# Optimization experiments

Hardware: AMD Instinct MI355X
Metric: run time of the kernel (lower is better)

The kernel has to match this reference:

```python
import math
import jax, jax.numpy as jnp
import numpy as np

N_HEAD = 8
BLOCK_SIZE = 1024
LN_EPS = 1e-5


def _layer_norm(x, g, b):
    mu = jnp.mean(x, axis=-1, keepdims=True)
    var = jnp.var(x, axis=-1, keepdims=True)
    return (x - mu) * jax.lax.rsqrt(var + LN_EPS) * g + b


def _skew(QEr):
    # QEr: (B, nh, L, L) -> pad one zero column on the left, reshape, drop first row
    B, nh, nr, nc = QEr.shape
    padded = jnp.pad(QEr, ((0, 0), (0, 0), (0, 0), (1, 0)))  # (B, nh, nr, nc+1)
    reshaped = padded.reshape(B, nh, nc + 1, nr)
    return reshaped[:, :, 1:, :]  # (B, nh, nr, nc)


def _attn(x, W_qkv, b_qkv, W_o, b_o, Er):
    B, L, D = x.shape
    hs = D // N_HEAD
    qkv = x @ W_qkv + b_qkv  # (B, L, 3D)
    q, k, v = jnp.split(qkv, 3, axis=-1)
    # (B, nh, L, hs)
    q = q.reshape(B, L, N_HEAD, hs).transpose(0, 2, 1, 3)
    k = k.reshape(B, L, N_HEAD, hs).transpose(0, 2, 1, 3)
    v = v.reshape(B, L, N_HEAD, hs).transpose(0, 2, 1, 3)
    start = BLOCK_SIZE - L
    Er_t = Er[start:, :].T  # (hs, L)
    QEr = q @ Er_t  # (B, nh, L, L)
    Srel = _skew(QEr)
    scores = (jnp.einsum('bhqd,bhkd->bhqk', q, k) + Srel) * (1.0 / math.sqrt(hs))
    causal = jnp.tril(jnp.ones((L, L), dtype=bool))
    scores = jnp.where(causal, scores, jnp.float32(-jnp.inf))
    att = jax.nn.softmax(scores, axis=-1)
    y = jnp.einsum('bhqk,bhkd->bhqd', att, v)
    y = y.transpose(0, 2, 1, 3).reshape(B, L, D)
    return y @ W_o + b_o


def reference(x, W_qkv, b_qkv, W_o, b_o, Er, ln1_g, ln1_b, ln2_g, ln2_b,
              W_fc, b_fc, W_proj, b_proj):
    x = x + _attn(_layer_norm(x, ln1_g, ln1_b), W_qkv, b_qkv, W_o, b_o, Er)
    h = _layer_norm(x, ln2_g, ln2_b) @ W_fc + b_fc
    h = jax.nn.gelu(h, approximate=False)
    h = h @ W_proj + b_proj
    return x + h


def setup_inputs() -> dict:
    key = jax.random.key(0)
    ks = jax.random.split(key, 8)
    B, L, D, F = 8, 1024, 1024, 4096
    hs = D // N_HEAD
    s = lambda fan_in: 1.0 / math.sqrt(fan_in)
    return {
        'x': jax.random.normal(ks[0], (B, L, D), dtype=jnp.float32),
        'W_qkv': jax.random.normal(ks[1], (D, 3 * D), dtype=jnp.float32) * s(D),
        'b_qkv': jnp.zeros((3 * D,), dtype=jnp.float32),
        'W_o': jax.random.normal(ks[2], (D, D), dtype=jnp.float32) * s(D),
        'b_o': jnp.zeros((D,), dtype=jnp.float32),
        'Er': jax.random.normal(ks[3], (BLOCK_SIZE, hs), dtype=jnp.float32),
        'ln1_g': jnp.ones((D,), dtype=jnp.float32),
        'ln1_b': jnp.zeros((D,), dtype=jnp.float32),
        'ln2_g': jnp.ones((D,), dtype=jnp.float32),
        'ln2_b': jnp.zeros((D,), dtype=jnp.float32),
        'W_fc': jax.random.normal(ks[4], (D, F), dtype=jnp.float32) * s(D),
        'b_fc': jnp.zeros((F,), dtype=jnp.float32),
        'W_proj': jax.random.normal(ks[5], (F, D), dtype=jnp.float32) * s(F),
        'b_proj': jnp.zeros((D,), dtype=jnp.float32),
    }
```

## Files before the change

kernel.cpp:

```cpp
#include <hip/hip_runtime.h>
#include <hip/hip_bf16.h>
#include <math.h>

#define BB 8
#define LL 1024
#define DD 1024
#define FF 4096
#define NHH 8
#define HSS 128
#define SCALE 0.08838834764831845f
#define TRI(qi, kt) ((qi) * ((qi) + 1) / 2 + (kt))

typedef __bf16 bf16;
typedef __bf16 bf16x8 __attribute__((ext_vector_type(8)));
typedef float f32x4 __attribute__((ext_vector_type(4)));
typedef _Float16 f16;
typedef _Float16 f16x4 __attribute__((ext_vector_type(4)));

__device__ inline void async_copy16(const void* g, void* l) {
  __builtin_amdgcn_global_load_lds(
      (const __attribute__((address_space(1))) unsigned int*)g,
      (__attribute__((address_space(3))) unsigned int*)l, 16, 0, 0);
}

__global__ __launch_bounds__(256)
void transpose_cast_kernel(const float* __restrict__ W, bf16* __restrict__ Wt,
                           int K, int N) {
  __shared__ float tile[32][33];
  int n0 = blockIdx.x * 32, k0 = blockIdx.y * 32;
  int tx = threadIdx.x, ty = threadIdx.y;
#pragma unroll
  for (int i = 0; i < 32; i += 8)
    tile[ty + i][tx] = W[(size_t)(k0 + ty + i) * N + n0 + tx];
  __syncthreads();
#pragma unroll
  for (int i = 0; i < 32; i += 8)
    Wt[(size_t)(n0 + ty + i) * K + k0 + tx] = (bf16)tile[tx][ty + i];
}

__global__ __launch_bounds__(256)
void cast_bf16_kernel(const float* __restrict__ src, bf16* __restrict__ dst, int n) {
  int i = blockIdx.x * blockDim.x + threadIdx.x;
  if (i < n) dst[i] = (bf16)src[i];
}

__global__ __launch_bounds__(256)
void ln_kernel(const float* __restrict__ x, const float* __restrict__ g,
               const float* __restrict__ bta, bf16* __restrict__ out) {
  int row = blockIdx.x;
  int tid = threadIdx.x;
  const float4 v = ((const float4*)(x + (size_t)row * DD))[tid];
  float s = v.x + v.y + v.z + v.w;
  float s2 = v.x * v.x + v.y * v.y + v.z * v.z + v.w * v.w;
#pragma unroll
  for (int o = 32; o > 0; o >>= 1) {
    s += __shfl_down(s, o);
    s2 += __shfl_down(s2, o);
  }
  __shared__ float a1[4], a2[4];
  int wave = tid >> 6;
  if ((tid & 63) == 0) { a1[wave] = s; a2[wave] = s2; }
  __syncthreads();
  s = a1[0] + a1[1] + a1[2] + a1[3];
  s2 = a2[0] + a2[1] + a2[2] + a2[3];
  float mu = s * (1.0f / DD);
  float rstd = rsqrtf(s2 * (1.0f / DD) - mu * mu + 1e-5f);
  float4 gv = ((const float4*)g)[tid];
  float4 bv = ((const float4*)bta)[tid];
  bf16* o4 = out + (size_t)row * DD + tid * 4;
  o4[0] = (bf16)((v.x - mu) * rstd * gv.x + bv.x);
  o4[1] = (bf16)((v.y - mu) * rstd * gv.y + bv.y);
  o4[2] = (bf16)((v.z - mu) * rstd * gv.z + bv.z);
  o4[3] = (bf16)((v.w - mu) * rstd * gv.w + bv.w);
}

template <int EPI>
__global__ __launch_bounds__(256)
void gemm_kernel(const bf16* __restrict__ A, const bf16* __restrict__ Bt,
                 const float* __restrict__ bias, const float* __restrict__ res,
                 void* __restrict__ Cout, int M, int N, int K) {
  __shared__ bf16 Als[128 * 32];
  __shared__ bf16 Bls[128 * 32];
  int tid = threadIdx.x;
  int wave = tid >> 6, lane = tid & 63;
  int l15 = lane & 15, quad = lane >> 4;
  int m0 = blockIdx.y * 128, n0 = blockIdx.x * 128;
  int wm = (wave >> 1) * 64, wn = (wave & 1) * 64;
  f32x4 acc[4][4] = {};

  for (int k0 = 0; k0 < K; k0 += 32) {
    __syncthreads();
#pragma unroll
    for (int i = 0; i < 2; i++) {
      int t = i * 256 + tid;
      int row = t >> 2, kc = (t & 3) << 3;
      async_copy16(A + (size_t)(m0 + row) * K + k0 + kc, &Als[t * 8]);
      async_copy16(Bt + (size_t)(n0 + row) * K + k0 + kc, &Bls[t * 8]);
    }
    __syncthreads();
    bf16x8 af[4], bfr[4];
#pragma unroll
    for (int mt = 0; mt < 4; mt++)
      af[mt] = *(const bf16x8*)&Als[(wm + mt * 16 + l15) * 32 + quad * 8];
#pragma unroll
    for (int nt = 0; nt < 4; nt++)
      bfr[nt] = *(const bf16x8*)&Bls[(wn + nt * 16 + l15) * 32 + quad * 8];
#pragma unroll
    for (int mt = 0; mt < 4; mt++)
#pragma unroll
      for (int nt = 0; nt < 4; nt++)
        acc[mt][nt] = __builtin_amdgcn_mfma_f32_16x16x32_bf16(af[mt], bfr[nt],
                                                              acc[mt][nt], 0, 0, 0);
  }

#pragma unroll
  for (int mt = 0; mt < 4; mt++) {
#pragma unroll
    for (int nt = 0; nt < 4; nt++) {
      int col = n0 + wn + nt * 16 + l15;
      float bv = bias[col];
#pragma unroll
      for (int r = 0; r < 4; r++) {
        int row = m0 + wm + mt * 16 + quad * 4 + r;
        float v = acc[mt][nt][r] + bv;
        if (EPI == 1) v = 0.5f * v * (1.0f + erff(v * 0.7071067811865475f));
        if (EPI == 2) {
          v += res[(size_t)row * N + col];
          ((float*)Cout)[(size_t)row * N + col] = v;
        } else {
          ((bf16*)Cout)[(size_t)row * N + col] = (bf16)v;
        }
      }
    }
  }
}

__global__ __launch_bounds__(256)
void pack_kv_kernel(const bf16* __restrict__ qkv, bf16* __restrict__ Kpack,
                    bf16* __restrict__ Vpack) {
  __shared__ bf16 Vst[64][132];
  int kt = blockIdx.x, h = blockIdx.y, b = blockIdx.z;
  int tid = threadIdx.x;
  const size_t rs = 3 * DD;
  const bf16* kb = qkv + (size_t)b * LL * rs + (size_t)(kt * 64) * rs + DD + h * HSS;
  const bf16* vb = kb + DD;
  bf16* kp = Kpack + ((size_t)(b * NHH + h) * 16 + kt) * (64 * 128);
  bf16* vp = Vpack + ((size_t)(b * NHH + h) * 16 + kt) * (128 * 64);
#pragma unroll
  for (int i = 0; i < 4; i++) {
    int u = i * 256 + tid;
    int kk = u >> 4, c = u & 15;
    bf16x8 kv = *(const bf16x8*)(kb + (size_t)kk * rs + c * 8);
    *(bf16x8*)(kp + kk * 128 + ((c ^ kk) & 15) * 8) = kv;
    *(bf16x8*)&Vst[kk][c * 8] = *(const bf16x8*)(vb + (size_t)kk * rs + c * 8);
  }
  __syncthreads();
#pragma unroll
  for (int i = 0; i < 4; i++) {
    int u = i * 256 + tid;
    int d = u >> 3, c = u & 7;
    bf16x8 t;
#pragma unroll
    for (int j = 0; j < 8; j++) t[j] = Vst[c * 8 + j][d];
    *(bf16x8*)(vp + d * 64 + ((c ^ (d & 7))) * 8) = t;
  }
}

__global__ __launch_bounds__(256)
void relband_kernel(const bf16* __restrict__ qkv, const bf16* __restrict__ Erb,
                    f16* __restrict__ band) {
  int t = blockIdx.x;
  int h = blockIdx.y, b = blockIdx.z;
  int qi = (int)((sqrtf((float)(8 * t + 1)) - 1.0f) * 0.5f);
  while (TRI(qi + 1, 0) <= t) qi++;
  while (TRI(qi, 0) > t) qi--;
  int kt = t - TRI(qi, 0);

  int tid = threadIdx.x, wave = tid >> 6, lane = tid & 63;
  int l15 = lane & 15, quad = lane >> 4;
  int qw0 = qi * 64 + wave * 16;
  int k0 = kt * 64;
  const size_t rs = 3 * DD;
  const bf16* qbase = qkv + (size_t)b * LL * rs + h * HSS;
  bf16x8 qf[4];
#pragma unroll
  for (int st = 0; st < 4; st++)
    qf[st] = *(const bf16x8*)(qbase + (size_t)(qw0 + l15) * rs + st * 32 + quad * 8);

  int kmax_off = qw0 + 15 - k0;
  int m_base = 1008 - qw0 + k0;
  int ntR = (kmax_off >> 4) + 1;
  if (ntR > 4) ntR = 4;
  f32x4 rr[5] = {};
#pragma unroll
  for (int n = 0; n < 5; n++) {
    if (n <= ntR) {
      int mr = m_base + n * 16 + l15;
      mr = mr < 0 ? 0 : (mr > 1023 ? 1023 : mr);
#pragma unroll
      for (int st = 0; st < 4; st++) {
        bf16x8 ef = *(const bf16x8*)(Erb + (size_t)mr * HSS + st * 32 + quad * 8);
        rr[n] = __builtin_amdgcn_mfma_f32_16x16x32_bf16(qf[st], ef, rr[n], 0, 0, 0);
      }
    }
  }
  f16x4 sf[4];
#pragma unroll
  for (int rg = 0; rg < 4; rg++) {
    int qloc = quad * 4 + rg;
    int tt = 15 - qloc + l15;
    int src = (lane & 48) | (tt & 15);
    float shv[5];
#pragma unroll
    for (int n = 0; n < 5; n++)
      shv[n] = (n <= ntR) ? __shfl(rr[n][rg], src) : 0.f;
#pragma unroll
    for (int nt = 0; nt < 4; nt++)
      sf[nt][rg] = (f16)((tt & 16) ? shv[nt + 1] : shv[nt]);
  }
  f16* tb = band + (size_t)(b * NHH + h) * (136 * 4096) + (size_t)t * 4096;
#pragma unroll
  for (int nt = 0; nt < 4; nt++)
    if (nt * 16 <= kmax_off)
      *(f16x4*)(tb + (wave * 4 + nt) * 256 + l15 * 16 + quad * 4) = sf[nt];
}

__global__ __launch_bounds__(256)
void flash_kernel(const bf16* __restrict__ qkv, const bf16* __restrict__ Kpack,
                  const bf16* __restrict__ Vpack, const f16* __restrict__ band,
                  bf16* __restrict__ y) {
  __shared__ bf16 Kls[2][64 * 128];
  __shared__ bf16 Vls[2][128 * 64];
  __shared__ bf16 Pls[4][16][72];

  int tid = threadIdx.x, wave = tid >> 6, lane = tid & 63;
  int l15 = lane & 15, quad = lane >> 4;
  int h = blockIdx.y, b = blockIdx.z;

  const size_t rs = 3 * DD;
  const bf16* qbase = qkv + (size_t)b * LL * rs + h * HSS;
  const bf16* kp = Kpack + (size_t)(b * NHH + h) * 16 * (64 * 128);
  const bf16* vp = Vpack + (size_t)(b * NHH + h) * 16 * (128 * 64);
  const f16* bnd = band + (size_t)(b * NHH + h) * (136 * 4096);

  int buf = 0;
#pragma unroll 1
  for (int ph = 0; ph < 2; ph++) {
    int qb = ph ? 15 - blockIdx.x : blockIdx.x;
    int qw0 = qb * 64 + wave * 16;
    int nkt = qb + 1;

    bf16x8 qf[4];
#pragma unroll
    for (int st = 0; st < 4; st++)
      qf[st] = *(const bf16x8*)(qbase + (size_t)(qw0 + l15) * rs + st * 32 + quad * 8);

    {
      const bf16* ks = kp;
      const bf16* vs = vp;
#pragma unroll
      for (int i = 0; i < 4; i++) {
        int off = (wave * 4 + i) * 512 + lane * 8;
        async_copy16(ks + off, &Kls[buf][off]);
        async_copy16(vs + off, &Vls[buf][off]);
      }
    }

    f32x4 o[8] = {};
    float mrow[4] = {-INFINITY, -INFINITY, -INFINITY, -INFINITY};
    float lrow[4] = {0.f, 0.f, 0.f, 0.f};

#pragma unroll 1
    for (int kt = 0; kt < nkt; kt++) {
      int k0 = kt * 64;
      int kmax_off = qw0 + 15 - k0;
      __syncthreads();

      const f16* tb = bnd + (size_t)TRI(qb, kt) * 4096;
      f16x4 srl[4] = {};
#pragma unroll
      for (int nt = 0; nt < 4; nt++)
        if (nt * 16 <= kmax_off)
          srl[nt] = *(const f16x4*)(tb + (wave * 4 + nt) * 256 + l15 * 16 + quad * 4);

      if (kt + 1 < nkt) {
        const bf16* ks = kp + (size_t)(kt + 1) * (64 * 128);
        const bf16* vs = vp + (size_t)(kt + 1) * (128 * 64);
#pragma unroll
        for (int i = 0; i < 4; i++) {
          int off = (wave * 4 + i) * 512 + lane * 8;
          async_copy16(ks + off, &Kls[buf ^ 1][off]);
          async_copy16(vs + off, &Vls[buf ^ 1][off]);
        }
      }

      f32x4 sa[4] = {};
#pragma unroll
      for (int nt = 0; nt < 4; nt++) {
        if (nt * 16 <= kmax_off) {
          int kk = nt * 16 + l15;
#pragma unroll
          for (int st = 0; st < 4; st++) {
            bf16x8 kf = *(const bf16x8*)&Kls[buf][kk * 128 + (((st * 4 + quad) ^ l15) & 15) * 8];
            sa[nt] = __builtin_amdgcn_mfma_f32_16x16x32_bf16(qf[st], kf, sa[nt], 0, 0, 0);
          }
        }
      }

      float pmx[4] = {-INFINITY, -INFINITY, -INFINITY, -INFINITY};
#pragma unroll
      for (int nt = 0; nt < 4; nt++) {
        if (nt * 16 <= kmax_off) {
          int kg = k0 + nt * 16 + l15;
#pragma unroll
          for (int rg = 0; rg < 4; rg++) {
            int qg = qw0 + quad * 4 + rg;
            float v = (sa[nt][rg] + (float)srl[nt][rg]) * SCALE;
            v = (kg <= qg) ? v : -INFINITY;
            sa[nt][rg] = v;
            pmx[rg] = fmaxf(pmx[rg], v);
          }
        } else {
#pragma unroll
          for (int rg = 0; rg < 4; rg++) sa[nt][rg] = -INFINITY;
        }
      }

#pragma unroll
      for (int rg = 0; rg < 4; rg++) {
        float v = pmx[rg];
        v = fmaxf(v, __shfl_xor(v, 1));
        v = fmaxf(v, __shfl_xor(v, 2));
        v = fmaxf(v, __shfl_xor(v, 4));
        v = fmaxf(v, __shfl_xor(v, 8));
        float mnew = fmaxf(mrow[rg], v);
        float alpha = __expf(mrow[rg] - mnew);
        mrow[rg] = mnew;
        lrow[rg] *= alpha;
#pragma unroll
        for (int nt = 0; nt < 8; nt++) o[nt][rg] *= alpha;
        pmx[rg] = mnew;
      }
      float ls[4] = {0.f, 0.f, 0.f, 0.f};
#pragma unroll
      for (int nt = 0; nt < 4; nt++)
#pragma unroll
        for (int rg = 0; rg < 4; rg++) {
          float p = __expf(sa[nt][rg] - pmx[rg]);
          ls[rg] += p;
          Pls[wave][quad * 4 + rg][nt * 16 + l15] = (bf16)p;
        }
#pragma unroll
      for (int rg = 0; rg < 4; rg++) {
        float v = ls[rg];
        v += __shfl_xor(v, 1);
        v += __shfl_xor(v, 2);
        v += __shfl_xor(v, 4);
        v += __shfl_xor(v, 8);
        lrow[rg] += v;
      }

      bf16x8 pf[2];
#pragma unroll
      for (int s2 = 0; s2 < 2; s2++)
        pf[s2] = *(const bf16x8*)&Pls[wave][l15][s2 * 32 + quad * 8];
#pragma unroll
      for (int nt = 0; nt < 8; nt++) {
        int d = nt * 16 + l15;
#pragma unroll
        for (int s2 = 0; s2 < 2; s2++) {
          if (s2 * 32 <= kmax_off) {
            bf16x8 vf = *(const bf16x8*)&Vls[buf][d * 64 + (((s2 * 4 + quad) ^ (l15 & 7)) & 7) * 8];
            o[nt] = __builtin_amdgcn_mfma_f32_16x16x32_bf16(pf[s2], vf, o[nt], 0, 0, 0);
          }
        }
      }
      buf ^= 1;
    }

#pragma unroll
    for (int rg = 0; rg < 4; rg++) {
      float inv = 1.0f / lrow[rg];
      int qg = qw0 + quad * 4 + rg;
      bf16* yr = y + ((size_t)b * LL + qg) * DD + h * HSS;
#pragma unroll
      for (int nt = 0; nt < 8; nt++) yr[nt * 16 + l15] = (bf16)(o[nt][rg] * inv);
    }
  }
}

extern "C" void kernel_launch(void* const* d_in, const int* in_sizes, int n_in,
                              void* d_out, int out_size, void* d_ws, size_t ws_size,
                              hipStream_t stream) {
  const float* x = (const float*)d_in[0];
  const float* W_qkv = (const float*)d_in[1];
  const float* b_qkv = (const float*)d_in[2];
  const float* W_o = (const float*)d_in[3];
  const float* b_o = (const float*)d_in[4];
  const float* Er = (const float*)d_in[5];
  const float* ln1_g = (const float*)d_in[6];
  const float* ln1_b = (const float*)d_in[7];
  const float* ln2_g = (const float*)d_in[8];
  const float* ln2_b = (const float*)d_in[9];
  const float* W_fc = (const float*)d_in[10];
  const float* b_fc = (const float*)d_in[11];
  const float* W_proj = (const float*)d_in[12];
  const float* b_proj = (const float*)d_in[13];
  float* out = (float*)d_out;

  char* p = (char*)d_ws;
  auto alloc = [&](size_t bytes) {
    char* r = p;
    p += (bytes + 255) & ~(size_t)255;
    return r;
  };
  bf16* Wt_qkv = (bf16*)alloc((size_t)3072 * 1024 * 2);
  bf16* Wt_o   = (bf16*)alloc((size_t)1024 * 1024 * 2);
  bf16* Wt_fc  = (bf16*)alloc((size_t)4096 * 1024 * 2);
  bf16* Wt_pr  = (bf16*)alloc((size_t)1024 * 4096 * 2);
  bf16* Erb    = (bf16*)alloc((size_t)1024 * 128 * 2);
  bf16* xn     = (bf16*)alloc((size_t)8192 * 1024 * 2);
  bf16* qkvb   = (bf16*)alloc((size_t)8192 * 3072 * 2);
  bf16* yb     = (bf16*)alloc((size_t)8192 * 1024 * 2);
  bf16* Kpack  = (bf16*)alloc((size_t)64 * 16 * 64 * 128 * 2);
  bf16* Vpack  = (bf16*)alloc((size_t)64 * 16 * 128 * 64 * 2);
  f16*  band   = (f16*)alloc((size_t)64 * 136 * 4096 * 2);
  float* x2    = (float*)band;
  bf16* hb     = qkvb;

  transpose_cast_kernel<<<dim3(3072 / 32, 1024 / 32), dim3(32, 8), 0, stream>>>(W_qkv, Wt_qkv, 1024, 3072);
  transpose_cast_kernel<<<dim3(1024 / 32, 1024 / 32), dim3(32, 8), 0, stream>>>(W_o, Wt_o, 1024, 1024);
  transpose_cast_kernel<<<dim3(4096 / 32, 1024 / 32), dim3(32, 8), 0, stream>>>(W_fc, Wt_fc, 1024, 4096);
  transpose_cast_kernel<<<dim3(1024 / 32, 4096 / 32), dim3(32, 8), 0, stream>>>(W_proj, Wt_pr, 4096, 1024);
  cast_bf16_kernel<<<512, 256, 0, stream>>>(Er, Erb, 1024 * 128);

  ln_kernel<<<8192, 256, 0, stream>>>(x, ln1_g, ln1_b, xn);
  gemm_kernel<0><<<dim3(24, 64), 256, 0, stream>>>(xn, Wt_qkv, b_qkv, nullptr, qkvb, 8192, 3072, 1024);
  pack_kv_kernel<<<dim3(16, 8, 8), 256, 0, stream>>>(qkvb, Kpack, Vpack);
  relband_kernel<<<dim3(136, 8, 8), 256, 0, stream>>>(qkvb, Erb, band);
  flash_kernel<<<dim3(8, 8, 8), 256, 0, stream>>>(qkvb, Kpack, Vpack, band, yb);
  gemm_kernel<2><<<dim3(8, 64), 256, 0, stream>>>(yb, Wt_o, b_o, x, x2, 8192, 1024, 1024);
  ln_kernel<<<8192, 256, 0, stream>>>(x2, ln2_g, ln2_b, xn);
  gemm_kernel<1><<<dim3(32, 64), 256, 0, stream>>>(xn, Wt_fc, b_fc, nullptr, hb, 8192, 4096, 1024);
  gemm_kernel<2><<<dim3(8, 64), 256, 0, stream>>>(hb, Wt_pr, b_proj, x2, out, 8192, 1024, 4096);
}
```

Before: 676.9 us.

## Double-buffer GEMM LDS tiles with K=64, XOR swizzle and block-id remapping

```diff
diff --git a/kernel.cpp b/kernel.cpp
--- a/kernel.cpp
+++ b/kernel.cpp
@@ -75,42 +75,74 @@
 }
 
 template <int EPI>
-__global__ __launch_bounds__(256)
+__global__ __launch_bounds__(256, 2)
 void gemm_kernel(const bf16* __restrict__ A, const bf16* __restrict__ Bt,
                  const float* __restrict__ bias, const float* __restrict__ res,
                  void* __restrict__ Cout, int M, int N, int K) {
-  __shared__ bf16 Als[128 * 32];
-  __shared__ bf16 Bls[128 * 32];
+  __shared__ bf16 Als[2][128 * 64];
+  __shared__ bf16 Bls[2][128 * 64];
   int tid = threadIdx.x;
   int wave = tid >> 6, lane = tid & 63;
   int l15 = lane & 15, quad = lane >> 4;
-  int m0 = blockIdx.y * 128, n0 = blockIdx.x * 128;
+
+  int gx = gridDim.x;
+  int nwg = gx * gridDim.y;
+  int id = blockIdx.y * gx + blockIdx.x;
+  int cpx = nwg >> 3;
+  int swz = (id & 7) * cpx + (id >> 3);
+  int bx = swz % gx, by = swz / gx;
+  int m0 = by * 128, n0 = bx * 128;
   int wm = (wave >> 1) * 64, wn = (wave & 1) * 64;
   f32x4 acc[4][4] = {};
 
-  for (int k0 = 0; k0 < K; k0 += 32) {
+  const bf16* asrc[4];
+  const bf16* bsrc[4];
+  int ldso[4];
+#pragma unroll
+  for (int i = 0; i < 4; i++) {
+    int u = i * 256 + tid;
+    int row = u >> 3, c = u & 7;
+    int g = c ^ (row & 7);
+    asrc[i] = A + (size_t)(m0 + row) * K + g * 8;
+    bsrc[i] = Bt + (size_t)(n0 + row) * K + g * 8;
+    ldso[i] = u * 8;
+  }
+
+  auto stage = [&](int bb, int k0) {
+#pragma unroll
+    for (int i = 0; i < 4; i++) {
+      async_copy16(asrc[i] + k0, &Als[bb][ldso[i]]);
+      async_copy16(bsrc[i] + k0, &Bls[bb][ldso[i]]);
+    }
+  };
+
+  stage(0, 0);
+  int nk = K >> 6;
+  int cur = 0;
+  for (int t = 0; t < nk; t++) {
     __syncthreads();
-#pragma unroll
-    for (int i = 0; i < 2; i++) {
-      int t = i * 256 + tid;
-      int row = t >> 2, kc = (t & 3) << 3;
-      async_copy16(A + (size_t)(m0 + row) * K + k0 + kc, &Als[t * 8]);
-      async_copy16(Bt + (size_t)(n0 + row) * K + k0 + kc, &Bls[t * 8]);
-    }
-    __syncthreads();
-    bf16x8 af[4], bfr[4];
-#pragma unroll
-    for (int mt = 0; mt < 4; mt++)
-      af[mt] = *(const bf16x8*)&Als[(wm + mt * 16 + l15) * 32 + quad * 8];
-#pragma unroll
-    for (int nt = 0; nt < 4; nt++)
-      bfr[nt] = *(const bf16x8*)&Bls[(wn + nt * 16 + l15) * 32 + quad * 8];
-#pragma unroll
-    for (int mt = 0; mt < 4; mt++)
-#pragma unroll
-      for (int nt = 0; nt < 4; nt++)
-        acc[mt][nt] = __builtin_amdgcn_mfma_f32_16x16x32_bf16(af[mt], bfr[nt],
-                                                              acc[mt][nt], 0, 0, 0);
+    if (t + 1 < nk) stage(cur ^ 1, (t + 1) << 6);
+
+    bf16x8 af[2][4], bfr[2][4];
+#pragma unroll
+    for (int kk = 0; kk < 2; kk++) {
+#pragma unroll
+      for (int mt = 0; mt < 4; mt++) {
+        int ra = wm + mt * 16 + l15;
+        af[kk][mt] = *(const bf16x8*)&Als[cur][ra * 64 + (((kk * 4 + quad) ^ (ra & 7)) << 3)];
+        int rb = wn + mt * 16 + l15;
+        bfr[kk][mt] = *(const bf16x8*)&Bls[cur][rb * 64 + (((kk * 4 + quad) ^ (rb & 7)) << 3)];
+      }
+    }
+#pragma unroll
+    for (int kk = 0; kk < 2; kk++)
+#pragma unroll
+      for (int mt = 0; mt < 4; mt++)
+#pragma unroll
+        for (int nt = 0; nt < 4; nt++)
+          acc[mt][nt] = __builtin_amdgcn_mfma_f32_16x16x32_bf16(af[kk][mt], bfr[kk][nt],
+                                                                acc[mt][nt], 0, 0, 0);
+    cur ^= 1;
   }
 
 #pragma unroll
```

Result: faster. 610.2 us (-9.9%).
